# Kernel tuning notes

Hardware: AMD Instinct MI355X
Metric: run time of the kernel (lower is better)

## Reference

```python
import jax, jax.numpy as jnp
import numpy as np

N = 8192
IN_DIM = 512
MEM_DIM = 512


def _linear_params(k, fan_in, fan_out):
    kw, kb = jax.random.split(k)
    s = 1.0 / np.sqrt(fan_in)
    W = jax.random.uniform(kw, (fan_in, fan_out), jnp.float32, -s, s)
    b = jax.random.uniform(kb, (fan_out,), jnp.float32, -s, s)
    return W, b


def setup_inputs() -> dict:
    key = jax.random.key(0)
    ks = jax.random.split(key, 12)
    inputs = jax.random.normal(ks[0], (N, IN_DIM), jnp.float32)
    # tree.type is a [1,2] mixing matrix per node (lang vs vis weights)
    type_mask = jax.nn.softmax(jax.random.normal(ks[1], (N, 2), jnp.float32), axis=-1)
    # topologically ordered tree: parent slot of node i is in [0, i]; slot 0 = virtual zero root state
    rng = np.random.default_rng(0)
    parent = np.zeros(N, dtype=np.int32)
    for i in range(1, N):
        parent[i] = rng.integers(0, i + 1)
    d = {"inputs": inputs, "type_mask": type_mask, "parent": jnp.asarray(parent)}
    names = ["ioux_vis", "iouh_vis", "fx_vis", "fh_vis",
             "ioux_lang", "iouh_lang", "fx_lang", "fh_lang"]
    fanins = [IN_DIM, MEM_DIM, IN_DIM, MEM_DIM] * 2
    fanouts = [3 * MEM_DIM, 3 * MEM_DIM, MEM_DIM, MEM_DIM] * 2
    for j, nm in enumerate(names):
        W, b = _linear_params(ks[2 + j], fanins[j], fanouts[j])
        d["W_" + nm] = W
        d["b_" + nm] = b
    return d


def reference(inputs, type_mask, parent,
              W_ioux_vis, b_ioux_vis, W_iouh_vis, b_iouh_vis,
              W_fx_vis, b_fx_vis, W_fh_vis, b_fh_vis,
              W_ioux_lang, b_ioux_lang, W_iouh_lang, b_iouh_lang,
              W_fx_lang, b_fx_lang, W_fh_lang, b_fh_lang):
    n_nodes = inputs.shape[0]
    D = W_fh_vis.shape[1]
    # batch the input-dependent projections into big GEMMs (fused across all nodes)
    x_iou_v = inputs @ W_ioux_vis + b_ioux_vis  # [N, 3D]
    x_f_v = inputs @ W_fx_vis + b_fx_vis        # [N, D]
    x_iou_l = inputs @ W_ioux_lang + b_ioux_lang
    x_f_l = inputs @ W_fx_lang + b_fx_lang

    def node(x_iou, x_f, h_p, c_p, W_iouh, b_iouh, W_fh, b_fh):
        iou = x_iou + h_p @ W_iouh + b_iouh  # [3D]
        i, o, u = jnp.split(iou, 3)
        f = jax.nn.sigmoid(x_f + h_p @ W_fh + b_fh)
        c = jax.nn.sigmoid(i) * jnp.tanh(u) + f * c_p
        h = jax.nn.sigmoid(o) * jnp.tanh(c)
        return c, h

    # slot 0 holds the zero state used by root nodes; node i lives at slot i+1
    c0 = jnp.zeros((n_nodes + 1, D), inputs.dtype)
    h0 = jnp.zeros((n_nodes + 1, D), inputs.dtype)

    def step(carry, xs):
        c_all, h_all = carry
        n, p, xiv, xfv, xil, xfl, tm = xs
        h_p = h_all[p]
        c_p = c_all[p]
        c_v, h_v = node(xiv, xfv, h_p, c_p, W_iouh_vis, b_iouh_vis, W_fh_vis, b_fh_vis)
        c_l, h_l = node(xil, xfl, h_p, c_p, W_iouh_lang, b_iouh_lang, W_fh_lang, b_fh_lang)
        # type_mask @ cat([lang, vis]) == tm[0]*lang + tm[1]*vis
        c_n = tm[0] * c_l + tm[1] * c_v
        h_n = tm[0] * h_l + tm[1] * h_v  # dropout is identity in eval
        return (c_all.at[n + 1].set(c_n), h_all.at[n + 1].set(h_n)), None

    idx = jnp.arange(n_nodes)
    (c_all, h_all), _ = jax.lax.scan(
        step, (c0, h0), (idx, parent, x_iou_v, x_f_v, x_iou_l, x_f_l, type_mask))
    return c_all[1:], h_all[1:]
```

## Files before the change

### kernel.cpp

```cpp
#include <hip/hip_runtime.h>
#include <math.h>

typedef unsigned short ushort_t;
typedef unsigned int uint_t;
typedef unsigned long long u64_t;
typedef __attribute__((ext_vector_type(8))) short short8;
typedef __attribute__((ext_vector_type(4))) float f32x4;

#define N_NODES 8192
#define DIM 512
#define KTOT 1024
#define NCOLS 4096
#define BM 128
#define BN 128
#define NTILE (NCOLS / BN)
#define KIT (KTOT / 32)
#define WIMG_USHORTS ((size_t)NTILE * KIT * 4096)
#define MAXLEV_LDS 128

__device__ __forceinline__ float sigm(float x) { return 1.0f / (1.0f + __expf(-x)); }
__device__ __forceinline__ float tanh_fast(float x) {
    float ax = fabsf(x);
    float e = __expf(2.0f * ax);
    float t = 1.0f - 2.0f / (e + 1.0f);
    return copysignf(t, x);
}
__device__ __forceinline__ uint_t packf(float f) {
    uint_t u = __float_as_uint(f);
    uint_t hi = u & 0xffff0000u;
    float r = f - __uint_as_float(hi);
    return hi | (__float_as_uint(r) >> 16);
}
__device__ __forceinline__ float unpackw(uint_t w) {
    return __uint_as_float(w & 0xffff0000u) + __uint_as_float(w << 16);
}
__device__ __forceinline__ uint_t rne16(float f) {
    uint_t u = __float_as_uint(f);
    return (u + 0x7fffu + ((u >> 16) & 1u)) >> 16;
}

__device__ __forceinline__ void fragAB_u32(const uint4 w0, const uint4 w1,
                                           short8& hi8, short8& lo8) {
    union { uint_t w[4]; short8 s; } H, L;
    uint_t u[8] = { w0.x, w0.y, w0.z, w0.w, w1.x, w1.y, w1.z, w1.w };
#pragma unroll
    for (int j = 0; j < 4; ++j) {
        H.w[j] = (u[2 * j + 1] & 0xffff0000u) | (u[2 * j] >> 16);
        L.w[j] = (u[2 * j + 1] << 16) | (u[2 * j] & 0xffffu);
    }
    hi8 = H.s; lo8 = L.s;
}

__device__ __forceinline__ void fragA_f32(const float4 f0, const float4 f1,
                                          short8& hi8, short8& lo8) {
    union { uint_t w[4]; short8 s; } H, L;
    float f[8] = { f0.x, f0.y, f0.z, f0.w, f1.x, f1.y, f1.z, f1.w };
#pragma unroll
    for (int j = 0; j < 4; ++j) {
        float a = f[2 * j], b = f[2 * j + 1];
        uint_t h0 = __float_as_uint(a) & 0xffff0000u;
        uint_t h1 = __float_as_uint(b) & 0xffff0000u;
        float r0 = a - __uint_as_float(h0);
        float r1 = b - __uint_as_float(h1);
        H.w[j] = h1 | (h0 >> 16);
        L.w[j] = (__float_as_uint(r1) & 0xffff0000u) | (__float_as_uint(r0) >> 16);
    }
    hi8 = H.s; lo8 = L.s;
}

__global__ void __launch_bounds__(256) prep_wimg_kernel(
    const float* __restrict__ Wx_iou_v, const float* __restrict__ Wh_iou_v,
    const float* __restrict__ Wx_f_v,   const float* __restrict__ Wh_f_v,
    const float* __restrict__ Wx_iou_l, const float* __restrict__ Wh_iou_l,
    const float* __restrict__ Wx_f_l,   const float* __restrict__ Wh_f_l,
    ushort_t* __restrict__ Wimg)
{
    __shared__ float T[32][132];
    int p = blockIdx.x >> 5, it = blockIdx.x & 31;
    int tid = threadIdx.x;
#pragma unroll
    for (int e = 0; e < 16; ++e) {
        int lin = e * 256 + tid;
        int dloc = lin & 15, kk = (lin >> 4) & 31, q = lin >> 9;
        int d = p * 16 + dloc;
        int qq = q & 3; bool lang = q >= 4;
        int k = it * 32 + kk;
        const float* W; int col, stride;
        if (qq < 3) { col = qq * DIM + d; stride = 3 * DIM;
            W = (k < DIM) ? (lang ? Wx_iou_l : Wx_iou_v) : (lang ? Wh_iou_l : Wh_iou_v); }
        else        { col = d; stride = DIM;
            W = (k < DIM) ? (lang ? Wx_f_l : Wx_f_v) : (lang ? Wh_f_l : Wh_f_v); }
        int kr = (k < DIM) ? k : (k - DIM);
        T[kk][dloc * 8 + q] = W[(size_t)kr * stride + col];
    }
    __syncthreads();
    size_t tilebase = (size_t)blockIdx.x * 4096;
#pragma unroll
    for (int gch = 0; gch < 2; ++gch) {
        int gi = gch * 256 + tid;
        int col = gi >> 2, gd = gi & 3;
        uint_t wds[4];
#pragma unroll
        for (int i = 0; i < 4; ++i) {
            uint_t v0 = rne16(T[gd * 8 + 2 * i][col]);
            uint_t v1 = rne16(T[gd * 8 + 2 * i + 1][col]);
            wds[i] = (v1 << 16) | v0;
        }
        *(uint4*)(Wimg + tilebase + (size_t)gi * 8) = make_uint4(wds[0], wds[1], wds[2], wds[3]);
    }
}

__global__ void prep_bias_kernel(
    const float* __restrict__ bx_iou_v, const float* __restrict__ bh_iou_v,
    const float* __restrict__ bx_f_v,   const float* __restrict__ bh_f_v,
    const float* __restrict__ bx_iou_l, const float* __restrict__ bh_iou_l,
    const float* __restrict__ bx_f_l,   const float* __restrict__ bh_f_l,
    float* __restrict__ bias)
{
    int j = blockIdx.x * blockDim.x + threadIdx.x;
    if (j >= NCOLS) return;
    int d = j >> 3, q = j & 7;
    int qq = q & 3;
    bool lang = (q & 4) != 0;
    const float* bx; const float* bh; int col;
    if (qq < 3) { col = qq * DIM + d; bx = lang ? bx_iou_l : bx_iou_v; bh = lang ? bh_iou_l : bh_iou_v; }
    else        { col = d;            bx = lang ? bx_f_l  : bx_f_v;   bh = lang ? bh_f_l  : bh_f_v; }
    bias[j] = bx[col] + bh[col];
}

__global__ void __launch_bounds__(1024) levels_sort_kernel(
    const int* __restrict__ parent,
    int* __restrict__ order, int* __restrict__ offsets,
    int* __restrict__ counts, int* __restrict__ cursors,
    int* __restrict__ nlev, int* __restrict__ tilestart,
    int* __restrict__ rbStart, int* __restrict__ nodeHrb)
{
    __shared__ int s_level[N_NODES];
    __shared__ int s_assigned;
    __shared__ int s_maxlev;
    int tid = threadIdx.x;
    int pr[8];
#pragma unroll
    for (int ii = 0; ii < 8; ++ii) {
        int i = tid + ii * 1024;
        pr[ii] = parent[i];
        s_level[i] = -1;
    }
    for (int i = tid; i <= N_NODES; i += 1024) counts[i] = 0;
    if (tid == 0) { s_assigned = 0; s_maxlev = 0; }
    __syncthreads();

    for (int pass = 0; pass <= N_NODES; ++pass) {
        int newly = 0;
#pragma unroll
        for (int ii = 0; ii < 8; ++ii) {
            int i = tid + ii * 1024;
            if (s_level[i] < 0) {
                int p = pr[ii];
                if (p == 0) { s_level[i] = 0; newly++; }
                else { int lp = s_level[p - 1]; if (lp >= 0) { s_level[i] = lp + 1; newly++; } }
            }
        }
        if (newly) atomicAdd(&s_assigned, newly);
        __syncthreads();
        int a = s_assigned;
        if (a >= N_NODES) break;
        __syncthreads();
    }

#pragma unroll
    for (int ii = 0; ii < 8; ++ii) {
        int i = tid + ii * 1024;
        int lv = s_level[i];
        atomicAdd(&counts[lv], 1);
        atomicMax(&s_maxlev, lv);
    }
    __syncthreads();
    if (tid == 0) {
        int nl = s_maxlev + 1;
        nlev[0] = nl;
        int off = 0, toff = 0, rb = 0;
        for (int l = 0; l < nl; ++l) {
            offsets[l] = off; cursors[l] = off;
            tilestart[l] = toff; rbStart[l] = rb;
            int mt = (counts[l] + BM - 1) / BM;
            rb += mt;
            toff += mt * NTILE;
            off += counts[l];
        }
        offsets[nl] = off;
        tilestart[nl] = toff;
        rbStart[nl] = rb;
        nlev[1] = toff;
    }
    __syncthreads();
#pragma unroll
    for (int ii = 0; ii < 8; ++ii) {
        int i = tid + ii * 1024;
        int lv = s_level[i];
        int pos = atomicAdd(&cursors[lv], 1);
        order[pos] = i;
        nodeHrb[i] = rbStart[lv] + ((pos - offsets[lv]) >> 7);
    }
}

__global__ void __launch_bounds__(512, 2) tree_fused_kernel(
    const float* __restrict__ inputs, const float* __restrict__ type_mask,
    const ushort_t* __restrict__ Wimg, const float* __restrict__ bias,
    const int* __restrict__ order, const int* __restrict__ offsets,
    const int* __restrict__ nlev, const int* __restrict__ parent,
    const int* __restrict__ rbStart,
    int* __restrict__ colCnt,
    uint_t* __restrict__ hPack, uint_t* __restrict__ cPack,
    float* __restrict__ out)
{
    float* cOut = out;
    float* hOut = out + (size_t)N_NODES * DIM;

    __shared__ float eps[BM * 132];
    __shared__ int s_node[BM];
    __shared__ int s_par[BM];
    __shared__ float s_tm[BM][2];
    __shared__ int s_rbs[MAXLEV_LDS];
    __shared__ int s_off[MAXLEV_LDS];

    int tid = threadIdx.x;
    int lane = tid & 63, w = tid >> 6;
    int wr = w >> 1, wc = w & 1;
    int l15 = lane & 15, g = lane >> 4;
    int nl = nlev[0];
    int total = nlev[1];

    int nload = nl + 1; if (nload > MAXLEV_LDS) nload = MAXLEV_LDS;
    for (int i = tid; i < nload; i += 512) { s_rbs[i] = rbStart[i]; s_off[i] = offsets[i]; }
    __syncthreads();

    const ushort_t* bLane = Wimg + (size_t)(wc * 64 + l15) * 32 + (size_t)g * 8;

#define LDB(RB, tilebase, itt) { \
    _Pragma("unroll") for (int n_ = 0; n_ < 4; ++n_) \
        RB[n_] = *(const uint4*)(bLane + (size_t)(tilebase + (itt)) * 4096 + n_ * 512); }

#define LDA_H(RA, itrel) { \
    _Pragma("unroll") for (int m_ = 0; m_ < 2; ++m_) { \
        const uint4* p_ = (const uint4*)(aBaseH[m_] + (itrel) * 32 + g * 8); \
        RA[m_][0] = p_[0]; RA[m_][1] = p_[1]; } }

#define LDA_X(RA, itt) { \
    _Pragma("unroll") for (int m_ = 0; m_ < 2; ++m_) { \
        const float4* p_ = (const float4*)(aBaseX[m_] + (itt) * 32 + g * 8); \
        RA[m_][0] = p_[0]; RA[m_][1] = p_[1]; } }

#define COMP_H(RA, RB) { \
    short8 bh_[4]; \
    _Pragma("unroll") for (int n_ = 0; n_ < 4; ++n_) { \
        union { uint4 u; short8 s; } c_; c_.u = RB[n_]; bh_[n_] = c_.s; } \
    _Pragma("unroll") for (int m_ = 0; m_ < 2; ++m_) { \
        short8 ah_, al_; fragAB_u32(RA[m_][0], RA[m_][1], ah_, al_); \
        _Pragma("unroll") for (int n_ = 0; n_ < 4; ++n_) { \
            acc[m_][n_] = __builtin_amdgcn_mfma_f32_16x16x32_bf16(ah_, bh_[n_], acc[m_][n_], 0, 0, 0); \
            acc[m_][n_] = __builtin_amdgcn_mfma_f32_16x16x32_bf16(al_, bh_[n_], acc[m_][n_], 0, 0, 0); } } }

#define COMP_X(RA, RB) { \
    short8 bh_[4]; \
    _Pragma("unroll") for (int n_ = 0; n_ < 4; ++n_) { \
        union { uint4 u; short8 s; } c_; c_.u = RB[n_]; bh_[n_] = c_.s; } \
    _Pragma("unroll") for (int m_ = 0; m_ < 2; ++m_) { \
        short8 ah_, al_; fragA_f32(RA[m_][0], RA[m_][1], ah_, al_); \
        _Pragma("unroll") for (int n_ = 0; n_ < 4; ++n_) { \
            acc[m_][n_] = __builtin_amdgcn_mfma_f32_16x16x32_bf16(ah_, bh_[n_], acc[m_][n_], 0, 0, 0); \
            acc[m_][n_] = __builtin_amdgcn_mfma_f32_16x16x32_bf16(al_, bh_[n_], acc[m_][n_], 0, 0, 0); } } }

#define POLL_ALL(colPrev, nPrev) { \
    int ok_ = 1; \
    if (lane < 32) { \
        int c_ = __hip_atomic_load(&(colPrev)[lane], __ATOMIC_RELAXED, \
                                   __HIP_MEMORY_SCOPE_AGENT); \
        ok_ = (c_ >= (nPrev)) ? 1 : 0; \
    } \
    uint_t cm_ = (uint_t)(__ballot(ok_) & 0xffffffffu); \
    uint_t gr_ = cm_ & (cm_ >> 1) & (cm_ >> 2) & (cm_ >> 3); \
    gmask = 0; \
    _Pragma("unroll") for (int g_ = 0; g_ < 8; ++g_) \
        gmask |= ((gr_ >> (4 * g_)) & 1u) << g_; }

#define WAVE_GATE(colPrev, nPrev, gq, slp) { \
    if (!(gmask & (1u << (gq)))) { \
        for (;;) { \
            POLL_ALL(colPrev, nPrev); \
            if (gmask & (1u << (gq))) break; \
            __builtin_amdgcn_s_sleep(slp); \
        } \
        asm volatile("" ::: "memory"); \
    } }

    for (int t = blockIdx.x; t < total; t += gridDim.x) {
        int lev = 0;
        while (lev + 1 < nload && s_rbs[lev + 1] * NTILE <= t) ++lev;
        int lt = t - s_rbs[lev] * NTILE;
        int ntile = lt % NTILE;
        int mt = lt / NTILE;
        int start = s_off[lev];
        int cnt = s_off[lev + 1] - start;
        int jc = ntile * BN;
        int r0 = mt * BM;
        int tbx = ntile * KIT;
        int tbh = ntile * KIT + 16;

        if (tid < BM) {
            int r = r0 + tid;
            int node = (r < cnt) ? order[start + r] : -1;
            s_node[tid] = node;
            int p = (node >= 0) ? parent[node] : 0;
            s_par[tid] = p;
            float t0 = 0.f, t1 = 0.f;
            if (node >= 0) { t0 = type_mask[node * 2]; t1 = type_mask[node * 2 + 1]; }
            s_tm[tid][0] = t0; s_tm[tid][1] = t1;
        }
        __syncthreads();

        f32x4 acc[2][4];
#pragma unroll
        for (int m = 0; m < 2; ++m)
#pragma unroll
            for (int n = 0; n < 4; ++n) acc[m][n] = (f32x4)(0.f);

        {
            const float* aBaseX[2];
#pragma unroll
            for (int m = 0; m < 2; ++m) {
                int nd = s_node[wr * 32 + m * 16 + l15];
                aBaseX[m] = inputs + (size_t)(nd < 0 ? 0 : nd) * DIM;
            }
            float4 xa0[2][2], xa1[2][2]; uint4 xb0[4], xb1[4];
            LDA_X(xa0, 0); LDB(xb0, tbx, 0);
            LDA_X(xa1, 1); LDB(xb1, tbx, 1);
#pragma unroll
            for (int ii = 0; ii < 8; ++ii) {
                int e = 2 * ii, o = e + 1;
                __builtin_amdgcn_s_setprio(1);
                COMP_X(xa0, xb0);
                __builtin_amdgcn_s_setprio(0);
                if (e + 2 < 16) { LDA_X(xa0, e + 2); LDB(xb0, tbx, e + 2); }
                __builtin_amdgcn_s_setprio(1);
                COMP_X(xa1, xb1);
                __builtin_amdgcn_s_setprio(0);
                if (o + 2 < 16) { LDA_X(xa1, o + 2); LDB(xb1, tbx, o + 2); }
            }
        }

        if (lev > 0) {
            const int* colPrev = colCnt + (lev - 1) * NTILE;
            int nPrev = s_rbs[lev] - s_rbs[lev - 1];
            const int gb = ntile >> 2;
            uint_t gmask = 0;

            const uint_t* aBaseH[2];
#pragma unroll
            for (int m = 0; m < 2; ++m) {
                int p = s_par[wr * 32 + m * 16 + l15];
                aBaseH[m] = hPack + (size_t)((p > 0) ? (p - 1) : 0) * DIM;
            }

            uint4 ha0[2][2], ha1[2][2]; uint4 hb0[4], hb1[4];
            WAVE_GATE(colPrev, nPrev, gb, 4);
            LDA_H(ha0, 2 * gb); LDB(hb0, tbh, 2 * gb);
            LDA_H(ha1, 2 * gb + 1); LDB(hb1, tbh, 2 * gb + 1);
#pragma unroll
            for (int s = 0; s < 8; ++s) {
                const int gn = (gb + s + 1) & 7;
                __builtin_amdgcn_s_setprio(1);
                COMP_H(ha0, hb0);
                __builtin_amdgcn_s_setprio(0);
                if (s < 7) {
                    WAVE_GATE(colPrev, nPrev, gn, 1);
                    LDA_H(ha0, 2 * gn); LDB(hb0, tbh, 2 * gn);
                }
                __builtin_amdgcn_s_setprio(1);
                COMP_H(ha1, hb1);
                __builtin_amdgcn_s_setprio(0);
                if (s < 7) { LDA_H(ha1, 2 * gn + 1); LDB(hb1, tbh, 2 * gn + 1); }
            }
        }

        int cntloc = cnt - r0; if (cntloc > BM) cntloc = BM;
        int erow = tid >> 2, qd = tid & 3;
        int dbase = (jc >> 3) + qd * 4;

        float CPv[4];
        {
            int p = (erow < cntloc) ? s_par[erow] : 0;
            uint4 cw = make_uint4(0u, 0u, 0u, 0u);
            if (p > 0) cw = *(const uint4*)(cPack + (size_t)(p - 1) * DIM + dbase);
            CPv[0] = unpackw(cw.x); CPv[1] = unpackw(cw.y);
            CPv[2] = unpackw(cw.z); CPv[3] = unpackw(cw.w);
        }

#pragma unroll
        for (int m = 0; m < 2; ++m)
#pragma unroll
            for (int n = 0; n < 4; ++n) {
                int row = wr * 32 + m * 16 + g * 4;
                int c = wc * 64 + n * 16 + l15;
#pragma unroll
                for (int r = 0; r < 4; ++r) eps[(row + r) * 132 + c] = acc[m][n][r];
            }
        __syncthreads();

        float cn4[4], hn4[4];
        int enode = -1;
        if (erow < cntloc) {
            enode = s_node[erow];
            const float* ep = &eps[erow * 132 + qd * 32];
            float tm0 = s_tm[erow][0], tm1 = s_tm[erow][1];
            float cpl[4] = { CPv[0], CPv[1], CPv[2], CPv[3] };
#pragma unroll
            for (int j = 0; j < 4; ++j) {
                float4 v0 = *(const float4*)(ep + j * 8);
                float4 v1 = *(const float4*)(ep + j * 8 + 4);
                int jb = jc + (qd * 4 + j) * 8;
                float4 b0 = *(const float4*)(bias + jb);
                float4 b1 = *(const float4*)(bias + jb + 4);
                float cp = cpl[j];
                float cv = sigm(v0.x + b0.x) * tanh_fast(v0.z + b0.z)
                         + sigm(v0.w + b0.w) * cp;
                float hv = sigm(v0.y + b0.y) * tanh_fast(cv);
                float cl = sigm(v1.x + b1.x) * tanh_fast(v1.z + b1.z)
                         + sigm(v1.w + b1.w) * cp;
                float hl = sigm(v1.y + b1.y) * tanh_fast(cl);
                cn4[j] = tm0 * cl + tm1 * cv;
                hn4[j] = tm0 * hl + tm1 * hv;
            }
            size_t oi = (size_t)enode * DIM + dbase;
            u64_t c01 = (u64_t)packf(cn4[0]) | ((u64_t)packf(cn4[1]) << 32);
            u64_t c23 = (u64_t)packf(cn4[2]) | ((u64_t)packf(cn4[3]) << 32);
            u64_t h01 = (u64_t)packf(hn4[0]) | ((u64_t)packf(hn4[1]) << 32);
            u64_t h23 = (u64_t)packf(hn4[2]) | ((u64_t)packf(hn4[3]) << 32);
            u64_t* cdst = (u64_t*)(cPack + oi);
            u64_t* hdst = (u64_t*)(hPack + oi);
            __hip_atomic_store(cdst,     c01, __ATOMIC_RELAXED, __HIP_MEMORY_SCOPE_AGENT);
            __hip_atomic_store(cdst + 1, c23, __ATOMIC_RELAXED, __HIP_MEMORY_SCOPE_AGENT);
            __hip_atomic_store(hdst,     h01, __ATOMIC_RELAXED, __HIP_MEMORY_SCOPE_AGENT);
            __hip_atomic_store(hdst + 1, h23, __ATOMIC_RELAXED, __HIP_MEMORY_SCOPE_AGENT);
        }

        __builtin_amdgcn_s_waitcnt(0);
        __syncthreads();
        if (tid == 0)
            __hip_atomic_fetch_add(&colCnt[lev * NTILE + ntile], 1,
                                   __ATOMIC_RELAXED, __HIP_MEMORY_SCOPE_AGENT);

        if (enode >= 0) {
            size_t oi = (size_t)enode * DIM + dbase;
            *(float4*)(cOut + oi) = make_float4(cn4[0], cn4[1], cn4[2], cn4[3]);
            *(float4*)(hOut + oi) = make_float4(hn4[0], hn4[1], hn4[2], hn4[3]);
        }
        __syncthreads();
    }
#undef LDB
#undef LDA_H
#undef LDA_X
#undef COMP_H
#undef COMP_X
#undef POLL_ALL
#undef WAVE_GATE
}

extern "C" void kernel_launch(void* const* d_in, const int* in_sizes, int n_in,
                              void* d_out, int out_size, void* d_ws, size_t ws_size,
                              hipStream_t stream) {
    const float* inputs      = (const float*)d_in[0];
    const float* type_mask   = (const float*)d_in[1];
    const int*   parent      = (const int*)d_in[2];
    const float* W_ioux_vis  = (const float*)d_in[3];
    const float* b_ioux_vis  = (const float*)d_in[4];
    const float* W_iouh_vis  = (const float*)d_in[5];
    const float* b_iouh_vis  = (const float*)d_in[6];
    const float* W_fx_vis    = (const float*)d_in[7];
    const float* b_fx_vis    = (const float*)d_in[8];
    const float* W_fh_vis    = (const float*)d_in[9];
    const float* b_fh_vis    = (const float*)d_in[10];
    const float* W_ioux_lang = (const float*)d_in[11];
    const float* b_ioux_lang = (const float*)d_in[12];
    const float* W_iouh_lang = (const float*)d_in[13];
    const float* b_iouh_lang = (const float*)d_in[14];
    const float* W_fx_lang   = (const float*)d_in[15];
    const float* b_fx_lang   = (const float*)d_in[16];
    const float* W_fh_lang   = (const float*)d_in[17];
    const float* b_fh_lang   = (const float*)d_in[18];

    ushort_t* Wimg = (ushort_t*)d_ws;
    float* bias    = (float*)(Wimg + WIMG_USHORTS);
    int* order     = (int*)(bias + NCOLS);
    int* offsets   = order + N_NODES;
    int* counts    = offsets + (N_NODES + 2);
    int* cursors   = counts + (N_NODES + 2);
    int* nlev      = cursors + (N_NODES + 2);
    int* tilestart = nlev + 8;
    int* rbStart   = tilestart + (N_NODES + 2);
    int* nodeHrb   = rbStart + (N_NODES + 2);
    int* colCnt    = nodeHrb + N_NODES;
    size_t off2 = (size_t)((char*)(colCnt + MAXLEV_LDS * NTILE) - (char*)d_ws);
    off2 = (off2 + 255) & ~(size_t)255;
    uint_t* hPack = (uint_t*)((char*)d_ws + off2);
    uint_t* cPack = hPack + (size_t)N_NODES * DIM;

    float* out = (float*)d_out;

    hipMemsetAsync((void*)colCnt, 0, MAXLEV_LDS * NTILE * sizeof(int), stream);

    hipLaunchKernelGGL(prep_wimg_kernel, dim3(NTILE * KIT), dim3(256), 0, stream,
                       W_ioux_vis, W_iouh_vis, W_fx_vis, W_fh_vis,
                       W_ioux_lang, W_iouh_lang, W_fx_lang, W_fh_lang, Wimg);
    hipLaunchKernelGGL(prep_bias_kernel, dim3(NCOLS / 256), dim3(256), 0, stream,
                       b_ioux_vis, b_iouh_vis, b_fx_vis, b_fh_vis,
                       b_ioux_lang, b_iouh_lang, b_fx_lang, b_fh_lang, bias);
    hipLaunchKernelGGL(levels_sort_kernel, dim3(1), dim3(1024), 0, stream,
                       parent, order, offsets, counts, cursors, nlev, tilestart,
                       rbStart, nodeHrb);

    int occ = 0;
    if (hipOccupancyMaxActiveBlocksPerMultiprocessor(&occ, (const void*)tree_fused_kernel, 512, 0) != hipSuccess || occ < 1)
        occ = 1;
    int bpc = occ < 2 ? occ : 2;
    dim3 grid(256 * bpc);

    void* args[] = { (void*)&inputs, (void*)&type_mask, (void*)&Wimg, (void*)&bias,
                     (void*)&order, (void*)&offsets, (void*)&nlev, (void*)&parent,
                     (void*)&rbStart, (void*)&colCnt,
                     (void*)&hPack, (void*)&cPack, (void*)&out };
    hipLaunchCooperativeKernel((const void*)tree_fused_kernel, grid, dim3(512), args, 0, stream);
}
```

Measured before the change: 774.3 us.

## Refine cross-level dependency gating to per-k-step granularity and split h/c readiness

Dependency polling now checks readiness per k-iteration (pairs of column tiles) rather than per group of four, so the recurrent GEMM can start as soon as its exact h slices are published. The h-part loop becomes a 16-step pipeline with a 3-deep A buffer and a 2-deep B buffer. The c state is now published after the h state, with a separate per-tile counter, and the epilogue waits only on the matching c column tile. The aim is to let blocks at the next tree level begin earlier, at the cost of extra counter atomics, a waitcnt and an extra barrier per tile.

```diff
diff --git a/kernel.cpp b/kernel.cpp
--- a/kernel.cpp
+++ b/kernel.cpp
@@ -210,7 +210,7 @@
     const int* __restrict__ order, const int* __restrict__ offsets,
     const int* __restrict__ nlev, const int* __restrict__ parent,
     const int* __restrict__ rbStart,
-    int* __restrict__ colCnt,
+    int* __restrict__ colCnt, int* __restrict__ cCnt,
     uint_t* __restrict__ hPack, uint_t* __restrict__ cPack,
     float* __restrict__ out)
 {
@@ -271,7 +271,7 @@
             acc[m_][n_] = __builtin_amdgcn_mfma_f32_16x16x32_bf16(ah_, bh_[n_], acc[m_][n_], 0, 0, 0); \
             acc[m_][n_] = __builtin_amdgcn_mfma_f32_16x16x32_bf16(al_, bh_[n_], acc[m_][n_], 0, 0, 0); } } }
 
-#define POLL_ALL(colPrev, nPrev) { \
+#define POLL16(colPrev, nPrev) { \
     int ok_ = 1; \
     if (lane < 32) { \
         int c_ = __hip_atomic_load(&(colPrev)[lane], __ATOMIC_RELAXED, \
@@ -279,16 +279,16 @@
         ok_ = (c_ >= (nPrev)) ? 1 : 0; \
     } \
     uint_t cm_ = (uint_t)(__ballot(ok_) & 0xffffffffu); \
-    uint_t gr_ = cm_ & (cm_ >> 1) & (cm_ >> 2) & (cm_ >> 3); \
-    gmask = 0; \
-    _Pragma("unroll") for (int g_ = 0; g_ < 8; ++g_) \
-        gmask |= ((gr_ >> (4 * g_)) & 1u) << g_; }
-
-#define WAVE_GATE(colPrev, nPrev, gq, slp) { \
-    if (!(gmask & (1u << (gq)))) { \
+    uint_t pr_ = cm_ & (cm_ >> 1); \
+    pmask = 0; \
+    _Pragma("unroll") for (int p_ = 0; p_ < 16; ++p_) \
+        pmask |= ((pr_ >> (2 * p_)) & 1u) << p_; }
+
+#define GATEI(colPrev, nPrev, itq, slp) { \
+    if (!(pmask & (1u << (itq)))) { \
         for (;;) { \
-            POLL_ALL(colPrev, nPrev); \
-            if (gmask & (1u << (gq))) break; \
+            POLL16(colPrev, nPrev); \
+            if (pmask & (1u << (itq))) break; \
             __builtin_amdgcn_s_sleep(slp); \
         } \
         asm volatile("" ::: "memory"); \
@@ -306,6 +306,7 @@
         int r0 = mt * BM;
         int tbx = ntile * KIT;
         int tbh = ntile * KIT + 16;
+        int nPrev = (lev > 0) ? (s_rbs[lev] - s_rbs[lev - 1]) : 0;
 
         if (tid < BM) {
             int r = r0 + tid;
@@ -351,9 +352,8 @@
 
         if (lev > 0) {
             const int* colPrev = colCnt + (lev - 1) * NTILE;
-            int nPrev = s_rbs[lev] - s_rbs[lev - 1];
-            const int gb = ntile >> 2;
-            uint_t gmask = 0;
+            const int it0 = ntile >> 1;
+            uint_t pmask = 0;
 
             const uint_t* aBaseH[2];
 #pragma unroll
@@ -362,31 +362,39 @@
                 aBaseH[m] = hPack + (size_t)((p > 0) ? (p - 1) : 0) * DIM;
             }
 
-            uint4 ha0[2][2], ha1[2][2]; uint4 hb0[4], hb1[4];
-            WAVE_GATE(colPrev, nPrev, gb, 4);
-            LDA_H(ha0, 2 * gb); LDB(hb0, tbh, 2 * gb);
-            LDA_H(ha1, 2 * gb + 1); LDB(hb1, tbh, 2 * gb + 1);
-#pragma unroll
-            for (int s = 0; s < 8; ++s) {
-                const int gn = (gb + s + 1) & 7;
+#define ITQ(s) ((it0 + (s)) & 15)
+            uint4 ha[3][2][2]; uint4 hb[2][4];
+            GATEI(colPrev, nPrev, ITQ(0), 2);
+            LDA_H(ha[0], ITQ(0)); LDB(hb[0], tbh, ITQ(0));
+            GATEI(colPrev, nPrev, ITQ(1), 1);
+            LDA_H(ha[1], ITQ(1)); LDB(hb[1], tbh, ITQ(1));
+            GATEI(colPrev, nPrev, ITQ(2), 1);
+            LDA_H(ha[2], ITQ(2));
+#pragma unroll
+            for (int s = 0; s < 16; ++s) {
                 __builtin_amdgcn_s_setprio(1);
-                COMP_H(ha0, hb0);
+                COMP_H(ha[s % 3], hb[s & 1]);
                 __builtin_amdgcn_s_setprio(0);
-                if (s < 7) {
-                    WAVE_GATE(colPrev, nPrev, gn, 1);
-                    LDA_H(ha0, 2 * gn); LDB(hb0, tbh, 2 * gn);
+                if (s + 3 < 16) {
+                    GATEI(colPrev, nPrev, ITQ(s + 3), 1);
+                    LDA_H(ha[s % 3], ITQ(s + 3));
                 }
-                __builtin_amdgcn_s_setprio(1);
-                COMP_H(ha1, hb1);
-                __builtin_amdgcn_s_setprio(0);
-                if (s < 7) { LDA_H(ha1, 2 * gn + 1); LDB(hb1, tbh, 2 * gn + 1); }
-            }
+                if (s + 2 < 16) { LDB(hb[s & 1], tbh, ITQ(s + 2)); }
+            }
+#undef ITQ
         }
 
         int cntloc = cnt - r0; if (cntloc > BM) cntloc = BM;
         int erow = tid >> 2, qd = tid & 3;
         int dbase = (jc >> 3) + qd * 4;
 
+        if (lev > 0) {
+            const int* cPrev = cCnt + (lev - 1) * NTILE;
+            while (__hip_atomic_load(&cPrev[ntile], __ATOMIC_RELAXED,
+                                     __HIP_MEMORY_SCOPE_AGENT) < nPrev)
+                __builtin_amdgcn_s_sleep(1);
+            asm volatile("" ::: "memory");
+        }
         float CPv[4];
         {
             int p = (erow < cntloc) ? s_par[erow] : 0;
@@ -432,14 +440,9 @@
                 hn4[j] = tm0 * hl + tm1 * hv;
             }
             size_t oi = (size_t)enode * DIM + dbase;
-            u64_t c01 = (u64_t)packf(cn4[0]) | ((u64_t)packf(cn4[1]) << 32);
-            u64_t c23 = (u64_t)packf(cn4[2]) | ((u64_t)packf(cn4[3]) << 32);
             u64_t h01 = (u64_t)packf(hn4[0]) | ((u64_t)packf(hn4[1]) << 32);
             u64_t h23 = (u64_t)packf(hn4[2]) | ((u64_t)packf(hn4[3]) << 32);
-            u64_t* cdst = (u64_t*)(cPack + oi);
             u64_t* hdst = (u64_t*)(hPack + oi);
-            __hip_atomic_store(cdst,     c01, __ATOMIC_RELAXED, __HIP_MEMORY_SCOPE_AGENT);
-            __hip_atomic_store(cdst + 1, c23, __ATOMIC_RELAXED, __HIP_MEMORY_SCOPE_AGENT);
             __hip_atomic_store(hdst,     h01, __ATOMIC_RELAXED, __HIP_MEMORY_SCOPE_AGENT);
             __hip_atomic_store(hdst + 1, h23, __ATOMIC_RELAXED, __HIP_MEMORY_SCOPE_AGENT);
         }
@@ -452,9 +455,19 @@
 
         if (enode >= 0) {
             size_t oi = (size_t)enode * DIM + dbase;
+            u64_t c01 = (u64_t)packf(cn4[0]) | ((u64_t)packf(cn4[1]) << 32);
+            u64_t c23 = (u64_t)packf(cn4[2]) | ((u64_t)packf(cn4[3]) << 32);
+            u64_t* cdst = (u64_t*)(cPack + oi);
+            __hip_atomic_store(cdst,     c01, __ATOMIC_RELAXED, __HIP_MEMORY_SCOPE_AGENT);
+            __hip_atomic_store(cdst + 1, c23, __ATOMIC_RELAXED, __HIP_MEMORY_SCOPE_AGENT);
             *(float4*)(cOut + oi) = make_float4(cn4[0], cn4[1], cn4[2], cn4[3]);
             *(float4*)(hOut + oi) = make_float4(hn4[0], hn4[1], hn4[2], hn4[3]);
         }
+        __builtin_amdgcn_s_waitcnt(0);
+        __syncthreads();
+        if (tid == 0)
+            __hip_atomic_fetch_add(&cCnt[lev * NTILE + ntile], 1,
+                                   __ATOMIC_RELAXED, __HIP_MEMORY_SCOPE_AGENT);
         __syncthreads();
     }
 #undef LDB
@@ -462,8 +475,8 @@
 #undef LDA_X
 #undef COMP_H
 #undef COMP_X
-#undef POLL_ALL
-#undef WAVE_GATE
+#undef POLL16
+#undef GATEI
 }
 
 extern "C" void kernel_launch(void* const* d_in, const int* in_sizes, int n_in,
@@ -500,14 +513,15 @@
     int* rbStart   = tilestart + (N_NODES + 2);
     int* nodeHrb   = rbStart + (N_NODES + 2);
     int* colCnt    = nodeHrb + N_NODES;
-    size_t off2 = (size_t)((char*)(colCnt + MAXLEV_LDS * NTILE) - (char*)d_ws);
+    int* cCnt      = colCnt + MAXLEV_LDS * NTILE;
+    size_t off2 = (size_t)((char*)(cCnt + MAXLEV_LDS * NTILE) - (char*)d_ws);
     off2 = (off2 + 255) & ~(size_t)255;
     uint_t* hPack = (uint_t*)((char*)d_ws + off2);
     uint_t* cPack = hPack + (size_t)N_NODES * DIM;
 
     float* out = (float*)d_out;
 
-    hipMemsetAsync((void*)colCnt, 0, MAXLEV_LDS * NTILE * sizeof(int), stream);
+    hipMemsetAsync((void*)colCnt, 0, 2 * MAXLEV_LDS * NTILE * sizeof(int), stream);
 
     hipLaunchKernelGGL(prep_wimg_kernel, dim3(NTILE * KIT), dim3(256), 0, stream,
                        W_ioux_vis, W_iouh_vis, W_fx_vis, W_fh_vis,
@@ -527,7 +541,7 @@
 
     void* args[] = { (void*)&inputs, (void*)&type_mask, (void*)&Wimg, (void*)&bias,
                      (void*)&order, (void*)&offsets, (void*)&nlev, (void*)&parent,
-                     (void*)&rbStart, (void*)&colCnt,
+                     (void*)&rbStart, (void*)&colCnt, (void*)&cCnt,
                      (void*)&hPack, (void*)&cPack, (void*)&out };
     hipLaunchCooperativeKernel((const void*)tree_fused_kernel, grid, dim3(512), args, 0, stream);
 }
```

Measured after the change: 783.7 us. About the same (+1.2%).
